# Optimization experiments

Measured on AMD Instinct MI355X. Metric: run time of the kernel, lower is better.

Reference implementation:

```python
import jax, jax.numpy as jnp
import numpy as np

R = 2            # interleaving factor (init kwarg r)
C = 16           # feature channels
N = 500_000      # number of sparse voxels
GRID = 256       # fine-grid extent per axis


def setup_inputs() -> dict:
    key = jax.random.key(0)
    kc, kf = jax.random.split(key)
    coords = jax.random.randint(kc, (N, 3), 0, GRID, dtype=jnp.int32)
    feats = jax.random.normal(kf, (N, C), dtype=jnp.float32)
    return {"feats": feats, "coords": coords}


def reference(feats, coords):
    # Sparse interleaving: group fine voxels into coarse voxels of size R^3,
    # scattering each point's C features into the slot given by its intra-cell offset.
    r2 = R * R
    r3 = r2 * R
    n = coords.shape[0]
    base = coords // R                      # [N,3] coarse voxel coords
    off = coords % R                        # [N,3] intra-cell offset
    offset_idx = off[:, 0] * r2 + off[:, 1] * R + off[:, 2]  # [N]

    # jit-compatible unique: fixed output size (worst case: all points distinct)
    unique_coords, inv = jnp.unique(base, axis=0, size=n, fill_value=-1,
                                    return_inverse=True)
    inv = inv.reshape(-1)                   # [N] row in aggregated output

    # target column = offset_idx*C + channel  (matches torch scatter_ layout)
    col = offset_idx[:, None] * C + jnp.arange(C, dtype=offset_idx.dtype)[None, :]  # [N,C]
    agg = jnp.zeros((n, C * r3), dtype=feats.dtype)
    agg = agg.at[inv[:, None], col].set(feats)
    return unique_coords.astype(jnp.int32), agg
```

## Files before the change

kernel.cpp:

```cpp
#include <hip/hip_runtime.h>


#define WORDS 65536u

typedef float v4f __attribute__((ext_vector_type(4)));

__global__ void mark_init_kernel(const int* __restrict__ coords,
                                 unsigned* __restrict__ bitmap,
                                 int* __restrict__ winner, int n) {
    int i = blockIdx.x * 256 + threadIdx.x;
    int nthreads = gridDim.x * 256;
    for (int s = i; s < 8 * n; s += nthreads) winner[s] = -1;
    if (i >= n) return;
    int cx = coords[3 * i], cy = coords[3 * i + 1], cz = coords[3 * i + 2];
    unsigned key = ((unsigned)(cx >> 1) << 14) | ((unsigned)(cy >> 1) << 7) |
                   (unsigned)(cz >> 1);
    atomicOr(&bitmap[key >> 5], 1u << (key & 31));
}

__global__ void scanall_kernel(const unsigned* __restrict__ bitmap,
                               unsigned* __restrict__ chunkExcl,
                               unsigned* __restrict__ U) {
    __shared__ unsigned sh[256];
    int t = threadIdx.x;
    unsigned s = 0;
    unsigned base = (unsigned)t * 256u;
#pragma unroll 8
    for (unsigned j = 0; j < 256u; ++j) s += __popc(bitmap[base + j]);
    unsigned x = s;
    sh[t] = x; __syncthreads();
    for (int d = 1; d < 256; d <<= 1) {
        unsigned y = (t >= d) ? sh[t - d] : 0u;
        __syncthreads();
        x += y; sh[t] = x; __syncthreads();
    }
    chunkExcl[t] = x - s;
    if (t == 255) *U = x;
}

__global__ void rank_coords_pad_kernel(const unsigned* __restrict__ bitmap,
                                       const unsigned* __restrict__ chunkExcl,
                                       const unsigned* __restrict__ U,
                                       unsigned* __restrict__ rank_base,
                                       float* __restrict__ coords_out, int n) {
    __shared__ unsigned sh[256];
    int t = threadIdx.x;
    unsigned w = blockIdx.x * 256 + t;
    unsigned word = bitmap[w];
    unsigned cnt = __popc(word);
    unsigned x = cnt;
    sh[t] = x; __syncthreads();
    for (int d = 1; d < 256; d <<= 1) {
        unsigned y = (t >= d) ? sh[t - d] : 0u;
        __syncthreads();
        x += y; sh[t] = x; __syncthreads();
    }
    unsigned rb = chunkExcl[blockIdx.x] + x - cnt;
    rank_base[w] = rb;
    while (word) {
        int k = __ffs(word) - 1;
        word &= word - 1;
        unsigned cell = w * 32u + (unsigned)k;
        coords_out[3 * rb + 0] = (float)(cell >> 14);
        coords_out[3 * rb + 1] = (float)((cell >> 7) & 127u);
        coords_out[3 * rb + 2] = (float)(cell & 127u);
        ++rb;
    }
    unsigned u = *U;
    int nthreads = gridDim.x * 256;
    for (unsigned i = u + w; i < (unsigned)n; i += nthreads) {
        coords_out[3 * i + 0] = -1.0f;
        coords_out[3 * i + 1] = -1.0f;
        coords_out[3 * i + 2] = -1.0f;
    }
}

__global__ void winner_kernel(const int* __restrict__ coords,
                              const unsigned* __restrict__ bitmap,
                              const unsigned* __restrict__ rank_base,
                              int* __restrict__ winner, int n) {
    int i = blockIdx.x * 256 + threadIdx.x;
    if (i >= n) return;
    int cx = coords[3 * i], cy = coords[3 * i + 1], cz = coords[3 * i + 2];
    unsigned key = ((unsigned)(cx >> 1) << 14) | ((unsigned)(cy >> 1) << 7) |
                   (unsigned)(cz >> 1);
    unsigned off = ((unsigned)(cx & 1) << 2) | ((unsigned)(cy & 1) << 1) |
                   (unsigned)(cz & 1);
    unsigned wd = key >> 5;
    unsigned r = rank_base[wd] + __popc(bitmap[wd] & ((1u << (key & 31)) - 1u));
    atomicMax(&winner[r * 8u + off], i);
}

__global__ void gather_kernel(const float* __restrict__ feats,
                              const int* __restrict__ winner,
                              float* __restrict__ agg, int total4) {
    int j = blockIdx.x * 256 + threadIdx.x;
    if (j >= total4) return;
    int slot = j >> 2;
    int c4 = j & 3;
    int w = __builtin_nontemporal_load(&winner[slot]);
    v4f v = (v4f)(0.f);
    if (w >= 0) v = ((const v4f*)feats)[(size_t)w * 4 + c4];
    __builtin_nontemporal_store(v, (v4f*)agg + j);
}

extern "C" void kernel_launch(void* const* d_in, const int* in_sizes, int n_in,
                              void* d_out, int out_size, void* d_ws, size_t ws_size,
                              hipStream_t stream) {
    const float* feats = (const float*)d_in[0];
    const int* coords  = (const int*)d_in[1];
    int n = in_sizes[1] / 3;

    float* out        = (float*)d_out;
    float* coords_out = out;
    float* agg        = out + (size_t)3 * n;

    unsigned* bitmap    = (unsigned*)d_ws;
    unsigned* rank_base = bitmap + WORDS;
    unsigned* chunkExcl = rank_base + WORDS;
    unsigned* U         = chunkExcl + 256;
    int*      winner    = (int*)(U + 4);

    (void)hipMemsetAsync(bitmap, 0, WORDS * sizeof(unsigned), stream);

    int nb = (n + 255) / 256;
    mark_init_kernel<<<nb, 256, 0, stream>>>(coords, bitmap, winner, n);
    scanall_kernel<<<1, 256, 0, stream>>>(bitmap, chunkExcl, U);
    rank_coords_pad_kernel<<<WORDS / 256, 256, 0, stream>>>(bitmap, chunkExcl, U,
                                                            rank_base, coords_out, n);
    winner_kernel<<<nb, 256, 0, stream>>>(coords, bitmap, rank_base, winner, n);
    int total4 = n * 32;
    gather_kernel<<<(total4 + 255) / 256, 256, 0, stream>>>(feats, winner, agg,
                                                            total4);
}
```

Baseline: 372.3 us.

## Index winners by dense cell key and fuse ranking with feature gather

The winner table is now keyed by the dense coarse-cell id instead of the compacted rank, so winners are resolved in the marking pass with atomicMax. That removes the separate winner kernel and its second read of the coordinates. Ranking, coordinate emission, feature gather and padding are fused into one kernel that walks the set bits of each block's bitmap words through shared memory. The scan now produces per-64-word chunk offsets to match the new block size. The cost is a much larger winner table (8 ints per possible cell) that must be memset every call, and sparser atomics and reads spread over that larger footprint.

Result: slower. 404.4 us (+8.6%).

```diff
diff --git a/kernel.cpp b/kernel.cpp
--- a/kernel.cpp
+++ b/kernel.cpp
@@ -2,20 +2,23 @@
 
 
 #define WORDS 65536u
+#define RBLOCKS 1024
+#define WPB 64u
 
 typedef float v4f __attribute__((ext_vector_type(4)));
 
-__global__ void mark_init_kernel(const int* __restrict__ coords,
-                                 unsigned* __restrict__ bitmap,
-                                 int* __restrict__ winner, int n) {
+__global__ void mark_kernel(const int* __restrict__ coords,
+                            unsigned* __restrict__ bitmap,
+                            int* __restrict__ winner, int n) {
     int i = blockIdx.x * 256 + threadIdx.x;
-    int nthreads = gridDim.x * 256;
-    for (int s = i; s < 8 * n; s += nthreads) winner[s] = -1;
     if (i >= n) return;
     int cx = coords[3 * i], cy = coords[3 * i + 1], cz = coords[3 * i + 2];
     unsigned key = ((unsigned)(cx >> 1) << 14) | ((unsigned)(cy >> 1) << 7) |
                    (unsigned)(cz >> 1);
+    unsigned off = ((unsigned)(cx & 1) << 2) | ((unsigned)(cy & 1) << 1) |
+                   (unsigned)(cz & 1);
     atomicOr(&bitmap[key >> 5], 1u << (key & 31));
+    atomicMax(&winner[key * 8u + off], i);
 }
 
 __global__ void scanall_kernel(const unsigned* __restrict__ bitmap,
@@ -23,10 +26,17 @@
                                unsigned* __restrict__ U) {
     __shared__ unsigned sh[256];
     int t = threadIdx.x;
+    unsigned base = (unsigned)t * 256u;
+    unsigned c[4];
     unsigned s = 0;
-    unsigned base = (unsigned)t * 256u;
+#pragma unroll
+    for (int q = 0; q < 4; ++q) {
+        unsigned cq = 0;
 #pragma unroll 8
-    for (unsigned j = 0; j < 256u; ++j) s += __popc(bitmap[base + j]);
+        for (int j = 0; j < 64; ++j) cq += __popc(bitmap[base + (unsigned)(q * 64 + j)]);
+        c[q] = cq;
+        s += cq;
+    }
     unsigned x = s;
     sh[t] = x; __syncthreads();
     for (int d = 1; d < 256; d <<= 1) {
@@ -34,74 +44,88 @@
         __syncthreads();
         x += y; sh[t] = x; __syncthreads();
     }
-    chunkExcl[t] = x - s;
+    unsigned excl = x - s;
+    chunkExcl[4 * t + 0] = excl;
+    chunkExcl[4 * t + 1] = excl + c[0];
+    chunkExcl[4 * t + 2] = excl + c[0] + c[1];
+    chunkExcl[4 * t + 3] = excl + c[0] + c[1] + c[2];
     if (t == 255) *U = x;
 }
 
-__global__ void rank_coords_pad_kernel(const unsigned* __restrict__ bitmap,
-                                       const unsigned* __restrict__ chunkExcl,
-                                       const unsigned* __restrict__ U,
-                                       unsigned* __restrict__ rank_base,
-                                       float* __restrict__ coords_out, int n) {
-    __shared__ unsigned sh[256];
+__global__ __launch_bounds__(256)
+void rank_gather_kernel(const unsigned* __restrict__ bitmap,
+                        const unsigned* __restrict__ chunkExcl,
+                        const unsigned* __restrict__ Uptr,
+                        const int* __restrict__ winner,
+                        const float* __restrict__ feats,
+                        float* __restrict__ coords_out,
+                        float* __restrict__ agg, int n) {
+    __shared__ unsigned shCell[WPB * 32u];
+    __shared__ unsigned shScan[WPB];
+    __shared__ unsigned shCount;
     int t = threadIdx.x;
-    unsigned w = blockIdx.x * 256 + t;
-    unsigned word = bitmap[w];
-    unsigned cnt = __popc(word);
+    unsigned wbase = blockIdx.x * WPB;
+    unsigned rbBase = chunkExcl[blockIdx.x];
+
+    unsigned word = 0, cnt = 0;
+    if (t < (int)WPB) {
+        word = bitmap[wbase + (unsigned)t];
+        cnt = __popc(word);
+        shScan[t] = cnt;
+    }
+    __syncthreads();
     unsigned x = cnt;
-    sh[t] = x; __syncthreads();
-    for (int d = 1; d < 256; d <<= 1) {
-        unsigned y = (t >= d) ? sh[t - d] : 0u;
+    for (int d = 1; d < (int)WPB; d <<= 1) {
+        unsigned y = (t < (int)WPB && t >= d) ? shScan[t - d] : 0u;
         __syncthreads();
-        x += y; sh[t] = x; __syncthreads();
+        if (t < (int)WPB) { x += y; shScan[t] = x; }
+        __syncthreads();
     }
-    unsigned rb = chunkExcl[blockIdx.x] + x - cnt;
-    rank_base[w] = rb;
-    while (word) {
-        int k = __ffs(word) - 1;
-        word &= word - 1;
-        unsigned cell = w * 32u + (unsigned)k;
-        coords_out[3 * rb + 0] = (float)(cell >> 14);
-        coords_out[3 * rb + 1] = (float)((cell >> 7) & 127u);
-        coords_out[3 * rb + 2] = (float)(cell & 127u);
-        ++rb;
+    if (t == (int)WPB - 1) shCount = x;
+    if (t < (int)WPB) {
+        unsigned listpos = x - cnt;
+        unsigned rb = rbBase + listpos;
+        unsigned wtmp = word;
+        while (wtmp) {
+            int k = __ffs(wtmp) - 1;
+            wtmp &= wtmp - 1;
+            unsigned cell = (wbase + (unsigned)t) * 32u + (unsigned)k;
+            shCell[listpos] = cell;
+            coords_out[3 * rb + 0] = (float)(cell >> 14);
+            coords_out[3 * rb + 1] = (float)((cell >> 7) & 127u);
+            coords_out[3 * rb + 2] = (float)(cell & 127u);
+            ++listpos; ++rb;
+        }
     }
-    unsigned u = *U;
-    int nthreads = gridDim.x * 256;
-    for (unsigned i = u + w; i < (unsigned)n; i += nthreads) {
-        coords_out[3 * i + 0] = -1.0f;
-        coords_out[3 * i + 1] = -1.0f;
-        coords_out[3 * i + 2] = -1.0f;
+    __syncthreads();
+    unsigned count = shCount;
+
+    const v4f* feats4 = (const v4f*)feats;
+    v4f* agg4 = (v4f*)agg;
+    int grp = t >> 5;
+    int lane = t & 31;
+    int off = lane >> 2;
+    int c4 = lane & 3;
+    for (unsigned idx = (unsigned)grp; idx < count; idx += 8u) {
+        unsigned cell = shCell[idx];
+        int w = winner[cell * 8u + (unsigned)off];
+        v4f v = (v4f)(0.f);
+        if (w >= 0) v = feats4[(size_t)w * 4 + c4];
+        __builtin_nontemporal_store(v, agg4 + (size_t)(rbBase + idx) * 32 + lane);
     }
-}
 
-__global__ void winner_kernel(const int* __restrict__ coords,
-                              const unsigned* __restrict__ bitmap,
-                              const unsigned* __restrict__ rank_base,
-                              int* __restrict__ winner, int n) {
-    int i = blockIdx.x * 256 + threadIdx.x;
-    if (i >= n) return;
-    int cx = coords[3 * i], cy = coords[3 * i + 1], cz = coords[3 * i + 2];
-    unsigned key = ((unsigned)(cx >> 1) << 14) | ((unsigned)(cy >> 1) << 7) |
-                   (unsigned)(cz >> 1);
-    unsigned off = ((unsigned)(cx & 1) << 2) | ((unsigned)(cy & 1) << 1) |
-                   (unsigned)(cz & 1);
-    unsigned wd = key >> 5;
-    unsigned r = rank_base[wd] + __popc(bitmap[wd] & ((1u << (key & 31)) - 1u));
-    atomicMax(&winner[r * 8u + off], i);
-}
-
-__global__ void gather_kernel(const float* __restrict__ feats,
-                              const int* __restrict__ winner,
-                              float* __restrict__ agg, int total4) {
-    int j = blockIdx.x * 256 + threadIdx.x;
-    if (j >= total4) return;
-    int slot = j >> 2;
-    int c4 = j & 3;
-    int w = __builtin_nontemporal_load(&winner[slot]);
-    v4f v = (v4f)(0.f);
-    if (w >= 0) v = ((const v4f*)feats)[(size_t)w * 4 + c4];
-    __builtin_nontemporal_store(v, (v4f*)agg + j);
+    unsigned Uv = *Uptr;
+    unsigned gid = blockIdx.x * 256u + (unsigned)t;
+    unsigned nth = gridDim.x * 256u;
+    for (unsigned r = Uv + gid; r < (unsigned)n; r += nth) {
+        coords_out[3 * r + 0] = -1.0f;
+        coords_out[3 * r + 1] = -1.0f;
+        coords_out[3 * r + 2] = -1.0f;
+    }
+    v4f z = (v4f)(0.f);
+    for (size_t j = (size_t)Uv * 32 + gid; j < (size_t)n * 32; j += nth) {
+        __builtin_nontemporal_store(z, agg4 + j);
+    }
 }
 
 extern "C" void kernel_launch(void* const* d_in, const int* in_sizes, int n_in,
@@ -116,20 +140,16 @@
     float* agg        = out + (size_t)3 * n;
 
     unsigned* bitmap    = (unsigned*)d_ws;
-    unsigned* rank_base = bitmap + WORDS;
-    unsigned* chunkExcl = rank_base + WORDS;
-    unsigned* U         = chunkExcl + 256;
+    unsigned* chunkExcl = bitmap + WORDS;
+    unsigned* U         = chunkExcl + 1024;
     int*      winner    = (int*)(U + 4);
 
     (void)hipMemsetAsync(bitmap, 0, WORDS * sizeof(unsigned), stream);
+    (void)hipMemsetAsync(winner, 0xFF, (size_t)WORDS * 32u * 8u * sizeof(int), stream);
 
     int nb = (n + 255) / 256;
-    mark_init_kernel<<<nb, 256, 0, stream>>>(coords, bitmap, winner, n);
+    mark_kernel<<<nb, 256, 0, stream>>>(coords, bitmap, winner, n);
     scanall_kernel<<<1, 256, 0, stream>>>(bitmap, chunkExcl, U);
-    rank_coords_pad_kernel<<<WORDS / 256, 256, 0, stream>>>(bitmap, chunkExcl, U,
-                                                            rank_base, coords_out, n);
-    winner_kernel<<<nb, 256, 0, stream>>>(coords, bitmap, rank_base, winner, n);
-    int total4 = n * 32;
-    gather_kernel<<<(total4 + 255) / 256, 256, 0, stream>>>(feats, winner, agg,
-                                                            total4);
+    rank_gather_kernel<<<RBLOCKS, 256, 0, stream>>>(bitmap, chunkExcl, U, winner,
+                                                    feats, coords_out, agg, n);
 }
```

## Index winners by coarse cell key to drop the separate winner pass

Applied to the files above, without the earlier changes.

The per-slot winner table is now indexed by coarse cell key (all 2M cells × 8 offsets) instead of by compacted rank. This lets the atomicMax run in the mark kernel and removes the separate winner kernel along with its second read of coords. The rank kernel writes a compacted cell list that the gather uses to look up winners, and the single-block popcount scan now reads uint4. In exchange, a 64 MB workspace region must be memset every call and the gather does an extra indirection per element.

Result: slower. 391.1 us (+5.0%).

```diff
diff --git a/kernel.cpp b/kernel.cpp
--- a/kernel.cpp
+++ b/kernel.cpp
@@ -2,20 +2,22 @@
 
 
 #define WORDS 65536u
+#define SENTINEL 0xFFFFFFFFu
 
 typedef float v4f __attribute__((ext_vector_type(4)));
 
-__global__ void mark_init_kernel(const int* __restrict__ coords,
-                                 unsigned* __restrict__ bitmap,
-                                 int* __restrict__ winner, int n) {
+__global__ void mark_kernel(const int* __restrict__ coords,
+                            unsigned* __restrict__ bitmap,
+                            unsigned* __restrict__ winner, int n) {
     int i = blockIdx.x * 256 + threadIdx.x;
-    int nthreads = gridDim.x * 256;
-    for (int s = i; s < 8 * n; s += nthreads) winner[s] = -1;
     if (i >= n) return;
     int cx = coords[3 * i], cy = coords[3 * i + 1], cz = coords[3 * i + 2];
     unsigned key = ((unsigned)(cx >> 1) << 14) | ((unsigned)(cy >> 1) << 7) |
                    (unsigned)(cz >> 1);
+    unsigned off = ((unsigned)(cx & 1) << 2) | ((unsigned)(cy & 1) << 1) |
+                   (unsigned)(cz & 1);
     atomicOr(&bitmap[key >> 5], 1u << (key & 31));
+    atomicMax(&winner[key * 8u + off], (unsigned)i + 1u);
 }
 
 __global__ void scanall_kernel(const unsigned* __restrict__ bitmap,
@@ -23,10 +25,14 @@
                                unsigned* __restrict__ U) {
     __shared__ unsigned sh[256];
     int t = threadIdx.x;
+    const uint4* b4 = (const uint4*)bitmap;
+    unsigned base = (unsigned)t * 64u;
     unsigned s = 0;
-    unsigned base = (unsigned)t * 256u;
 #pragma unroll 8
-    for (unsigned j = 0; j < 256u; ++j) s += __popc(bitmap[base + j]);
+    for (unsigned j = 0; j < 64u; ++j) {
+        uint4 v = b4[base + j];
+        s += __popc(v.x) + __popc(v.y) + __popc(v.z) + __popc(v.w);
+    }
     unsigned x = s;
     sh[t] = x; __syncthreads();
     for (int d = 1; d < 256; d <<= 1) {
@@ -38,11 +44,12 @@
     if (t == 255) *U = x;
 }
 
-__global__ void rank_coords_pad_kernel(const unsigned* __restrict__ bitmap,
-                                       const unsigned* __restrict__ chunkExcl,
-                                       const unsigned* __restrict__ U,
-                                       unsigned* __restrict__ rank_base,
-                                       float* __restrict__ coords_out, int n) {
+__global__ __launch_bounds__(256)
+void rank_kernel(const unsigned* __restrict__ bitmap,
+                 const unsigned* __restrict__ chunkExcl,
+                 const unsigned* __restrict__ Uptr,
+                 unsigned* __restrict__ cells,
+                 float* __restrict__ coords_out, int n) {
     __shared__ unsigned sh[256];
     int t = threadIdx.x;
     unsigned w = blockIdx.x * 256 + t;
@@ -56,51 +63,44 @@
         x += y; sh[t] = x; __syncthreads();
     }
     unsigned rb = chunkExcl[blockIdx.x] + x - cnt;
-    rank_base[w] = rb;
     while (word) {
         int k = __ffs(word) - 1;
         word &= word - 1;
         unsigned cell = w * 32u + (unsigned)k;
+        cells[rb] = cell;
         coords_out[3 * rb + 0] = (float)(cell >> 14);
         coords_out[3 * rb + 1] = (float)((cell >> 7) & 127u);
         coords_out[3 * rb + 2] = (float)(cell & 127u);
         ++rb;
     }
-    unsigned u = *U;
-    int nthreads = gridDim.x * 256;
-    for (unsigned i = u + w; i < (unsigned)n; i += nthreads) {
-        coords_out[3 * i + 0] = -1.0f;
-        coords_out[3 * i + 1] = -1.0f;
-        coords_out[3 * i + 2] = -1.0f;
+    unsigned Uv = *Uptr;
+    unsigned gid = blockIdx.x * 256u + (unsigned)t;
+    unsigned nth = gridDim.x * 256u;
+    for (unsigned r = Uv + gid; r < (unsigned)n; r += nth) {
+        cells[r] = SENTINEL;
+        coords_out[3 * r + 0] = -1.0f;
+        coords_out[3 * r + 1] = -1.0f;
+        coords_out[3 * r + 2] = -1.0f;
     }
 }
 
-__global__ void winner_kernel(const int* __restrict__ coords,
-                              const unsigned* __restrict__ bitmap,
-                              const unsigned* __restrict__ rank_base,
-                              int* __restrict__ winner, int n) {
-    int i = blockIdx.x * 256 + threadIdx.x;
-    if (i >= n) return;
-    int cx = coords[3 * i], cy = coords[3 * i + 1], cz = coords[3 * i + 2];
-    unsigned key = ((unsigned)(cx >> 1) << 14) | ((unsigned)(cy >> 1) << 7) |
-                   (unsigned)(cz >> 1);
-    unsigned off = ((unsigned)(cx & 1) << 2) | ((unsigned)(cy & 1) << 1) |
-                   (unsigned)(cz & 1);
-    unsigned wd = key >> 5;
-    unsigned r = rank_base[wd] + __popc(bitmap[wd] & ((1u << (key & 31)) - 1u));
-    atomicMax(&winner[r * 8u + off], i);
-}
-
 __global__ void gather_kernel(const float* __restrict__ feats,
-                              const int* __restrict__ winner,
+                              const unsigned* __restrict__ winner,
+                              const unsigned* __restrict__ cells,
                               float* __restrict__ agg, int total4) {
     int j = blockIdx.x * 256 + threadIdx.x;
     if (j >= total4) return;
-    int slot = j >> 2;
-    int c4 = j & 3;
-    int w = __builtin_nontemporal_load(&winner[slot]);
+    unsigned row = (unsigned)j >> 5;
+    unsigned cell = cells[row];
     v4f v = (v4f)(0.f);
-    if (w >= 0) v = ((const v4f*)feats)[(size_t)w * 4 + c4];
+    if (cell != SENTINEL) {
+        unsigned off = ((unsigned)j >> 2) & 7u;
+        unsigned w = winner[cell * 8u + off];
+        if (w) {
+            unsigned c4 = (unsigned)j & 3u;
+            v = ((const v4f*)feats)[(size_t)(w - 1u) * 4u + c4];
+        }
+    }
     __builtin_nontemporal_store(v, (v4f*)agg + j);
 }
 
@@ -116,20 +116,20 @@
     float* agg        = out + (size_t)3 * n;
 
     unsigned* bitmap    = (unsigned*)d_ws;
-    unsigned* rank_base = bitmap + WORDS;
-    unsigned* chunkExcl = rank_base + WORDS;
+    unsigned* winner    = bitmap + WORDS;
+    unsigned* chunkExcl = winner + (size_t)WORDS * 256u;
     unsigned* U         = chunkExcl + 256;
-    int*      winner    = (int*)(U + 4);
+    unsigned* cells     = U + 4;
 
-    (void)hipMemsetAsync(bitmap, 0, WORDS * sizeof(unsigned), stream);
+    (void)hipMemsetAsync(d_ws, 0, (size_t)(WORDS + (size_t)WORDS * 256u) * 4u,
+                         stream);
 
     int nb = (n + 255) / 256;
-    mark_init_kernel<<<nb, 256, 0, stream>>>(coords, bitmap, winner, n);
+    mark_kernel<<<nb, 256, 0, stream>>>(coords, bitmap, winner, n);
     scanall_kernel<<<1, 256, 0, stream>>>(bitmap, chunkExcl, U);
-    rank_coords_pad_kernel<<<WORDS / 256, 256, 0, stream>>>(bitmap, chunkExcl, U,
-                                                            rank_base, coords_out, n);
-    winner_kernel<<<nb, 256, 0, stream>>>(coords, bitmap, rank_base, winner, n);
+    rank_kernel<<<WORDS / 256, 256, 0, stream>>>(bitmap, chunkExcl, U, cells,
+                                                 coords_out, n);
     int total4 = n * 32;
-    gather_kernel<<<(total4 + 255) / 256, 256, 0, stream>>>(feats, winner, agg,
-                                                            total4);
+    gather_kernel<<<(total4 + 255) / 256, 256, 0, stream>>>(feats, winner, cells,
+                                                            agg, total4);
 }
```
